# Kernel optimization log

Hardware: AMD Instinct MI355X
Metric: run time of the kernel (lower is better)

Reference implementation:

```python
import jax, jax.numpy as jnp
import numpy as np
from functools import partial

N_NODES = 50000
BN_EPS = 1e-5


def _renumber(src, dst, mask, n_nodes):
    # Faithful to extract_batch_edge_idx: kept edges are relabeled by the rank of
    # their node id among the sorted unique node ids APPEARING in kept edges.
    m = mask.astype(jnp.int32)
    appear = jnp.zeros(n_nodes, jnp.int32)
    appear = appear.at[src].max(m)
    appear = appear.at[dst].max(m)
    new_id = jnp.cumsum(appear) - 1  # rank of each appearing node id
    s = jnp.where(mask, new_id[src], 0)
    d = jnp.where(mask, new_id[dst], 0)
    return s, d


def _gcn_conv(x, W, b, src, dst, ew, n):
    # PyG GCNConv: linear, add self-loops, symmetric normalization, scatter-add.
    xw = x @ W                                   # [n, out]
    deg = jax.ops.segment_sum(ew, dst, num_segments=n) + 1.0  # +1 self loop
    dinv = jax.lax.rsqrt(deg)
    norm = dinv[src] * dinv[dst] * ew            # masked edges -> 0 weight
    agg = jax.ops.segment_sum(norm[:, None] * xw[src], dst, num_segments=n)
    agg = agg + (dinv * dinv)[:, None] * xw      # self-loop contribution
    return agg + b


def setup_inputs() -> dict:
    key = jax.random.key(0)
    ks = jax.random.split(key, 8)
    R, N, E, B = 3, N_NODES, 1000000, 2048
    inp, hid, out = 256, 512, 256
    features = jax.random.normal(ks[0], (R, N, inp), jnp.float32)
    W1 = jax.random.normal(ks[1], (inp, hid), jnp.float32) * (1.0 / np.sqrt(inp))
    b1 = jnp.zeros((hid,), jnp.float32)
    W2 = jax.random.normal(ks[2], (hid, out), jnp.float32) * (1.0 / np.sqrt(hid))
    b2 = jnp.zeros((out,), jnp.float32)
    gamma = jnp.ones((hid,), jnp.float32)
    beta = jnp.zeros((hid,), jnp.float32)
    edge_index = jax.random.randint(ks[3], (R, 2, E), 0, N, jnp.int64)
    # distinct, sorted batch node ids (torch code iterates node values)
    batch_nodes = jnp.sort(jax.random.permutation(ks[4], N)[:B]).astype(jnp.int64)
    return {"features": features, "W1": W1, "b1": b1, "W2": W2, "b2": b2,
            "gamma": gamma, "beta": beta, "edge_index": edge_index,
            "batch_nodes": batch_nodes}


def reference(features, W1, b1, W2, b2, gamma, beta, edge_index, batch_nodes):
    R, N, _ = features.shape
    B = batch_nodes.shape[0]
    in_batch = jnp.zeros(N, bool).at[batch_nodes].set(True)
    outs = []
    for r in range(R):  # small fixed relation count
        src, dst = edge_index[r, 0], edge_index[r, 1]
        mask = in_batch[src] & in_batch[dst]
        ew = mask.astype(features.dtype)
        s, d = _renumber(src, dst, mask, N)
        x = features[r, batch_nodes]             # [B, inp]
        h = _gcn_conv(x, W1, b1, s, d, ew, B)    # [B, hid]
        # BatchNorm1d (training mode: biased batch stats)
        mu = h.mean(axis=0)
        var = h.var(axis=0)
        h = (h - mu) * jax.lax.rsqrt(var + BN_EPS) * gamma + beta
        outs.append(_gcn_conv(h, W2, b2, s, d, ew, B))  # [B, out]
    stacked = jnp.stack(outs, axis=0)            # [R, B, out]
    return stacked.reshape(B, -1)                # row-major reshape, as torch
```

## Files before the change

kernel.cpp:

```cpp
#include <hip/hip_runtime.h>
#include <hip/hip_bf16.h>
#include <stdint.h>
#include <stddef.h>

#define RNUM   3
#define NNODES 50000
#define ENUM   1000000
#define BATCH  2048
#define INP    256
#define HID    512
#define OUTC   256
#define BN_EPS 1e-5f

typedef __bf16 bf16x8 __attribute__((ext_vector_type(8)));
typedef float  f32x4  __attribute__((ext_vector_type(4)));

__device__ inline unsigned short f2bf(float f) {
    union { float f; unsigned u; } c; c.f = f;
    unsigned u = c.u;
    return (unsigned short)((u + 0x7fffu + ((u >> 16) & 1u)) >> 16);
}

__device__ inline uint4 pack8(float4 a, float4 b) {
    uint4 r;
    r.x = (unsigned)f2bf(a.x) | ((unsigned)f2bf(a.y) << 16);
    r.y = (unsigned)f2bf(a.z) | ((unsigned)f2bf(a.w) << 16);
    r.z = (unsigned)f2bf(b.x) | ((unsigned)f2bf(b.y) << 16);
    r.w = (unsigned)f2bf(b.z) | ((unsigned)f2bf(b.w) << 16);
    return r;
}

__global__ __launch_bounds__(256) void k_wt(const float* __restrict__ W1,
                                            const float* __restrict__ W2,
                                            unsigned short* __restrict__ W1T,
                                            unsigned short* __restrict__ W2T) {
    __shared__ float T[32][33];
    int z = blockIdx.z;
    const float* W = z ? W2 : W1;
    unsigned short* WT = z ? W2T : W1T;
    int K = z ? HID : INP;
    int N = z ? OUTC : HID;
    int kt = blockIdx.y, nt = blockIdx.x;
    if (kt * 32 >= K || nt * 32 >= N) return;
    int tx = threadIdx.x & 31, ty = threadIdx.x >> 5;
#pragma unroll
    for (int j = 0; j < 4; ++j)
        T[ty + j * 8][tx] = W[(size_t)(kt * 32 + ty + j * 8) * N + nt * 32 + tx];
    __syncthreads();
#pragma unroll
    for (int j = 0; j < 4; ++j)
        WT[(size_t)(nt * 32 + ty + j * 8) * K + kt * 32 + tx] = f2bf(T[tx][ty + j * 8]);
}

__global__ void k_prep(const int* __restrict__ bn, int* __restrict__ inv,
                       int* __restrict__ appear, float* __restrict__ deg,
                       float* __restrict__ musum, float* __restrict__ sqsum,
                       int* __restrict__ kcount) {
    int i = blockIdx.x * blockDim.x + threadIdx.x;
    if (i < NNODES) {
        int lo = 0, hi = BATCH;
        while (lo < hi) { int mid = (lo + hi) >> 1; if (bn[mid] < i) lo = mid + 1; else hi = mid; }
        inv[i] = (lo < BATCH && bn[lo] == i) ? lo : -1;
    }
    if (i < RNUM * BATCH) { appear[i] = 0; deg[i] = 0.0f; }
    if (i < RNUM * HID)   { musum[i] = 0.0f; sqsum[i] = 0.0f; }
    if (i < RNUM)         kcount[i] = 0;
}

__global__ void k_mask(const int* __restrict__ edge_index, const int* __restrict__ inv,
                       int* __restrict__ appear, int2* __restrict__ edges,
                       int* __restrict__ kcount) {
    int z = blockIdx.z;
    const int* src = edge_index + (size_t)z * 2 * ENUM;
    const int* dst = src + ENUM;
    int2* ed = edges + (size_t)z * ENUM;
    int* app = appear + z * BATCH;
    int stride = gridDim.x * blockDim.x;
    for (int e4 = blockIdx.x * blockDim.x + threadIdx.x; e4 < ENUM / 4; e4 += stride) {
        int4 s4 = ((const int4*)src)[e4];
        int4 d4 = ((const int4*)dst)[e4];
        int ss[4] = {s4.x, s4.y, s4.z, s4.w};
        int dd[4] = {d4.x, d4.y, d4.z, d4.w};
#pragma unroll
        for (int i = 0; i < 4; ++i) {
            int ps = inv[ss[i]];
            int pd = inv[dd[i]];
            if (ps >= 0 && pd >= 0) {
                int idx = atomicAdd(kcount + z, 1);
                ed[idx] = make_int2(ps, pd);
                app[ps] = 1;
                app[pd] = 1;
            }
        }
    }
}

__global__ __launch_bounds__(1024) void k_scanDeg(const int* __restrict__ appear,
                                                  int2* __restrict__ edges,
                                                  const int* __restrict__ kcount,
                                                  float* __restrict__ deg) {
    __shared__ int buf[2][BATCH];
    __shared__ float degs[BATCH];
    int z = blockIdx.x;
    const int* ap = appear + z * BATCH;
    int2* ed = edges + (size_t)z * ENUM;
    float* dg = deg + z * BATCH;
    int t = threadIdx.x;
    buf[0][t] = ap[t];
    buf[0][t + 1024] = ap[t + 1024];
    degs[t] = 0.0f; degs[t + 1024] = 0.0f;
    __syncthreads();
    int cur = 0;
    for (int off = 1; off < BATCH; off <<= 1) {
        int nxt = cur ^ 1;
        int i1 = t, i2 = t + 1024;
        buf[nxt][i1] = buf[cur][i1] + (i1 >= off ? buf[cur][i1 - off] : 0);
        buf[nxt][i2] = buf[cur][i2] + (i2 >= off ? buf[cur][i2 - off] : 0);
        __syncthreads();
        cur = nxt;
    }
    int K = kcount[z];
    for (int e = t; e < K; e += 1024) {
        int2 E = ed[e];
        int s = buf[cur][E.x] - 1;
        int d = buf[cur][E.y] - 1;
        ed[e] = make_int2(s, d);
        atomicAdd(&degs[d], 1.0f);
    }
    __syncthreads();
    dg[t] = degs[t];
    dg[t + 1024] = degs[t + 1024];
}

__global__ __launch_bounds__(256) void k_gemm1(
    const float* __restrict__ features, const int* __restrict__ bn,
    const unsigned short* __restrict__ W1T, const float* __restrict__ b1,
    const float* __restrict__ deg, float* __restrict__ xw, float* __restrict__ hbase) {
    __shared__ __align__(16) unsigned short As[64][40];
    __shared__ __align__(16) unsigned short Bs[64][40];
    int z = blockIdx.z;
    const float* feat = features + (size_t)z * NNODES * INP;
    const float* dgz = deg + z * BATCH;
    float* xwz = xw + (size_t)z * BATCH * HID;
    float* hbz = hbase + (size_t)z * BATCH * HID;
    int m0 = blockIdx.y * 64, n0 = blockIdx.x * 64;
    int t = threadIdx.x;
    int ar = t >> 2, aq = t & 3;
    int grow = bn[m0 + ar];
    const float* aptr = feat + (size_t)grow * INP + aq * 8;
    const unsigned short* bptr = W1T + (size_t)(n0 + ar) * INP + aq * 8;

    int lane = t & 63, wave = t >> 6;
    int wm = (wave & 1) * 32, wn = (wave >> 1) * 32;
    int ml = lane & 15, quad = lane >> 4, q8 = quad * 8;

    f32x4 acc[2][2] = {};
    for (int k0 = 0; k0 < INP; k0 += 32) {
        float4 a0 = *(const float4*)(aptr + k0);
        float4 a1 = *(const float4*)(aptr + k0 + 4);
        uint4 bv = *(const uint4*)(bptr + k0);
        *(uint4*)&As[ar][aq * 8] = pack8(a0, a1);
        *(uint4*)&Bs[ar][aq * 8] = bv;
        __syncthreads();
        bf16x8 af[2], bfr[2];
#pragma unroll
        for (int mi = 0; mi < 2; ++mi) af[mi]  = *(const bf16x8*)&As[wm + mi * 16 + ml][q8];
#pragma unroll
        for (int ni = 0; ni < 2; ++ni) bfr[ni] = *(const bf16x8*)&Bs[wn + ni * 16 + ml][q8];
#pragma unroll
        for (int mi = 0; mi < 2; ++mi)
#pragma unroll
            for (int ni = 0; ni < 2; ++ni)
                acc[mi][ni] = __builtin_amdgcn_mfma_f32_16x16x32_bf16(af[mi], bfr[ni], acc[mi][ni], 0, 0, 0);
        __syncthreads();
    }
#pragma unroll
    for (int mi = 0; mi < 2; ++mi)
#pragma unroll
        for (int r = 0; r < 4; ++r) {
            int row = m0 + wm + mi * 16 + quad * 4 + r;
            float d2 = 1.0f / (dgz[row] + 1.0f);
#pragma unroll
            for (int ni = 0; ni < 2; ++ni) {
                int col = n0 + wn + ni * 16 + ml;
                float c = acc[mi][ni][r];
                xwz[(size_t)row * HID + col] = c;
                hbz[(size_t)row * HID + col] = d2 * c + b1[col];
            }
        }
}

__global__ __launch_bounds__(256) void k_gemm2(
    const float* __restrict__ hbase, const float* __restrict__ musum,
    const float* __restrict__ sqsum, const float* __restrict__ gamma,
    const float* __restrict__ beta, const unsigned short* __restrict__ W2T,
    const float* __restrict__ b2, const float* __restrict__ deg,
    float* __restrict__ yw, float* __restrict__ out) {
    __shared__ __align__(16) unsigned short As[64][40];
    __shared__ __align__(16) unsigned short Bs[64][40];
    __shared__ __align__(16) float gs[HID];
    __shared__ __align__(16) float ss_[HID];
    int z = blockIdx.z;
    const float* hz = hbase + (size_t)z * BATCH * HID;
    const float* dgz = deg + z * BATCH;
    float* ywz = yw + (size_t)z * BATCH * OUTC;
    float* oz = out + (size_t)z * BATCH * OUTC;
    int m0 = blockIdx.y * 64, n0 = blockIdx.x * 64;
    int t = threadIdx.x;

#pragma unroll
    for (int c = t; c < HID; c += 256) {
        float mu = musum[z * HID + c] * (1.0f / BATCH);
        float ex2 = sqsum[z * HID + c] * (1.0f / BATCH);
        float var = ex2 - mu * mu;
        float g = rsqrtf(var + BN_EPS) * gamma[c];
        gs[c] = g;
        ss_[c] = beta[c] - mu * g;
    }
    __syncthreads();

    int ar = t >> 2, aq = t & 3;
    const float* aptr = hz + (size_t)(m0 + ar) * HID + aq * 8;
    const unsigned short* bptr = W2T + (size_t)(n0 + ar) * HID + aq * 8;

    int lane = t & 63, wave = t >> 6;
    int wm = (wave & 1) * 32, wn = (wave >> 1) * 32;
    int ml = lane & 15, quad = lane >> 4, q8 = quad * 8;

    f32x4 acc[2][2] = {};
    for (int k0 = 0; k0 < HID; k0 += 32) {
        float4 h0 = *(const float4*)(aptr + k0);
        float4 h1 = *(const float4*)(aptr + k0 + 4);
        float4 g0 = *(const float4*)(gs + k0 + aq * 8);
        float4 g1 = *(const float4*)(gs + k0 + aq * 8 + 4);
        float4 s0 = *(const float4*)(ss_ + k0 + aq * 8);
        float4 s1 = *(const float4*)(ss_ + k0 + aq * 8 + 4);
        float4 a0 = make_float4(h0.x * g0.x + s0.x, h0.y * g0.y + s0.y,
                                h0.z * g0.z + s0.z, h0.w * g0.w + s0.w);
        float4 a1 = make_float4(h1.x * g1.x + s1.x, h1.y * g1.y + s1.y,
                                h1.z * g1.z + s1.z, h1.w * g1.w + s1.w);
        uint4 bv = *(const uint4*)(bptr + k0);
        *(uint4*)&As[ar][aq * 8] = pack8(a0, a1);
        *(uint4*)&Bs[ar][aq * 8] = bv;
        __syncthreads();
        bf16x8 af[2], bfr[2];
#pragma unroll
        for (int mi = 0; mi < 2; ++mi) af[mi]  = *(const bf16x8*)&As[wm + mi * 16 + ml][q8];
#pragma unroll
        for (int ni = 0; ni < 2; ++ni) bfr[ni] = *(const bf16x8*)&Bs[wn + ni * 16 + ml][q8];
#pragma unroll
        for (int mi = 0; mi < 2; ++mi)
#pragma unroll
            for (int ni = 0; ni < 2; ++ni)
                acc[mi][ni] = __builtin_amdgcn_mfma_f32_16x16x32_bf16(af[mi], bfr[ni], acc[mi][ni], 0, 0, 0);
        __syncthreads();
    }
#pragma unroll
    for (int mi = 0; mi < 2; ++mi)
#pragma unroll
        for (int r = 0; r < 4; ++r) {
            int row = m0 + wm + mi * 16 + quad * 4 + r;
            float d2 = 1.0f / (dgz[row] + 1.0f);
#pragma unroll
            for (int ni = 0; ni < 2; ++ni) {
                int col = n0 + wn + ni * 16 + ml;
                float c = acc[mi][ni][r];
                ywz[(size_t)row * OUTC + col] = c;
                oz[(size_t)row * OUTC + col] = d2 * c + b2[col];
            }
        }
}

__global__ void k_agg(const int2* __restrict__ edges, const int* __restrict__ kcount,
                      const float* __restrict__ deg, const float* __restrict__ src_mat,
                      float* __restrict__ dst_mat, int ncol) {
    int z = blockIdx.z;
    int K = kcount[z];
    const int2* ed = edges + (size_t)z * ENUM;
    const float* dgz = deg + z * BATCH;
    const float* sm = src_mat + (size_t)z * BATCH * ncol;
    float* dm = dst_mat + (size_t)z * BATCH * ncol;
    int nq = ncol >> 2;
    for (int e = blockIdx.x; e < K; e += gridDim.x) {
        int2 E = ed[e];
        float w = rsqrtf(dgz[E.x] + 1.0f) * rsqrtf(dgz[E.y] + 1.0f);
        const float4* srow = (const float4*)(sm + (size_t)E.x * ncol);
        float* drow = dm + (size_t)E.y * ncol;
        for (int q = threadIdx.x; q < nq; q += blockDim.x) {
            float4 v = srow[q];
            atomicAdd(&drow[q * 4 + 0], w * v.x);
            atomicAdd(&drow[q * 4 + 1], w * v.y);
            atomicAdd(&drow[q * 4 + 2], w * v.z);
            atomicAdd(&drow[q * 4 + 3], w * v.w);
        }
    }
}

__global__ __launch_bounds__(256) void k_bnstats(const float* __restrict__ hbase,
                                                 float* __restrict__ musum,
                                                 float* __restrict__ sqsum) {
    int z = blockIdx.z;
    const float* h = hbase + (size_t)z * BATCH * HID;
    int c0 = threadIdx.x;
    int r0 = blockIdx.x * 32;
    float s1a = 0, s2a = 0, s1b = 0, s2b = 0;
    for (int rr = 0; rr < 32; ++rr) {
        const float* row = h + (size_t)(r0 + rr) * HID;
        float va = row[c0];
        float vb = row[c0 + 256];
        s1a += va; s2a += va * va;
        s1b += vb; s2b += vb * vb;
    }
    atomicAdd(&musum[z * HID + c0], s1a);       atomicAdd(&sqsum[z * HID + c0], s2a);
    atomicAdd(&musum[z * HID + c0 + 256], s1b); atomicAdd(&sqsum[z * HID + c0 + 256], s2b);
}

extern "C" void kernel_launch(void* const* d_in, const int* in_sizes, int n_in,
                              void* d_out, int out_size, void* d_ws, size_t ws_size,
                              hipStream_t stream) {
    const float* features    = (const float*)d_in[0];
    const float* W1          = (const float*)d_in[1];
    const float* b1          = (const float*)d_in[2];
    const float* W2          = (const float*)d_in[3];
    const float* b2          = (const float*)d_in[4];
    const float* gamma       = (const float*)d_in[5];
    const float* beta        = (const float*)d_in[6];
    const int*   edge_index  = (const int*)d_in[7];
    const int*   batch_nodes = (const int*)d_in[8];
    float* out = (float*)d_out;

    char* p = (char*)d_ws;
    size_t cur = 0;
    auto alloc = [&](size_t bytes) {
        void* r = p + cur;
        cur = (cur + bytes + 255) & ~(size_t)255;
        return r;
    };
    int*   inv    = (int*)  alloc(NNODES * sizeof(int));
    int*   appear = (int*)  alloc(RNUM * BATCH * sizeof(int));
    int*   kcount = (int*)  alloc(RNUM * sizeof(int));
    float* deg    = (float*)alloc(RNUM * BATCH * sizeof(float));
    float* musum  = (float*)alloc(RNUM * HID * sizeof(float));
    float* sqsum  = (float*)alloc(RNUM * HID * sizeof(float));
    unsigned short* W1T = (unsigned short*)alloc((size_t)HID * INP * sizeof(unsigned short));
    unsigned short* W2T = (unsigned short*)alloc((size_t)OUTC * HID * sizeof(unsigned short));
    int2*  edges  = (int2*) alloc((size_t)RNUM * ENUM * sizeof(int2));
    float* xw     = (float*)alloc((size_t)RNUM * BATCH * HID * sizeof(float));
    float* hbase  = (float*)alloc((size_t)RNUM * BATCH * HID * sizeof(float));
    float* yw     = (float*)alloc((size_t)RNUM * BATCH * OUTC * sizeof(float));
    (void)ws_size; (void)in_sizes; (void)n_in; (void)out_size;

    k_wt<<<dim3(16, 16, 2), 256, 0, stream>>>(W1, W2, W1T, W2T);
    k_prep<<<(NNODES + 255) / 256, 256, 0, stream>>>(batch_nodes, inv, appear, deg,
                                                     musum, sqsum, kcount);
    k_mask<<<dim3(512, 1, RNUM), 256, 0, stream>>>(edge_index, inv, appear, edges, kcount);
    k_scanDeg<<<RNUM, 1024, 0, stream>>>(appear, edges, kcount, deg);

    k_gemm1<<<dim3(HID / 64, BATCH / 64, RNUM), 256, 0, stream>>>(
        features, batch_nodes, W1T, b1, deg, xw, hbase);
    k_agg<<<dim3(256, 1, RNUM), 256, 0, stream>>>(edges, kcount, deg, xw, hbase, HID);

    k_bnstats<<<dim3(64, 1, RNUM), 256, 0, stream>>>(hbase, musum, sqsum);

    k_gemm2<<<dim3(OUTC / 64, BATCH / 64, RNUM), 256, 0, stream>>>(
        hbase, musum, sqsum, gamma, beta, W2T, b2, deg, yw, out);
    k_agg<<<dim3(256, 1, RNUM), 256, 0, stream>>>(edges, kcount, deg, yw, out, OUTC);
}
```

Baseline: 365.6 us.

## Aggregate before linear layers, fold BN shift into correction vector, fuse stats

Reorders each GCN layer so neighbour aggregation runs on the narrower input (256 columns of features) before the first GEMM, and on the pre-BN hidden state before the second GEMM. The BatchNorm affine is applied through a per-node coefficient vector (sum of edge norms plus self-loop term) times shift@W2. BN statistics are now accumulated in the GEMM1 epilogue, so the separate stats pass and the second aggregation on GEMM outputs go away. Weight transpose and prep are merged into one launch that also zeroes the aggregation buffers. The cost is extra zero-fill traffic and a per-block 512-length dot product in GEMM2. The edge-parallel aggregations still rely on float atomics.

Measured after the change: 401.0 us. 9.7% more time.

```diff
diff --git a/kernel.cpp b/kernel.cpp
--- a/kernel.cpp
+++ b/kernel.cpp
@@ -30,41 +30,47 @@
     return r;
 }
 
-__global__ __launch_bounds__(256) void k_wt(const float* __restrict__ W1,
-                                            const float* __restrict__ W2,
-                                            unsigned short* __restrict__ W1T,
-                                            unsigned short* __restrict__ W2T) {
+__global__ __launch_bounds__(256) void k_prep(
+    const float* __restrict__ W1, const float* __restrict__ W2,
+    const int* __restrict__ bn,
+    unsigned short* __restrict__ W1T, unsigned short* __restrict__ W2T,
+    int* __restrict__ inv, int* __restrict__ appear, int* __restrict__ kcount,
+    float* __restrict__ musum, float* __restrict__ sqsum,
+    float* __restrict__ xa, float* __restrict__ ha) {
     __shared__ float T[32][33];
-    int z = blockIdx.z;
-    const float* W = z ? W2 : W1;
-    unsigned short* WT = z ? W2T : W1T;
-    int K = z ? HID : INP;
-    int N = z ? OUTC : HID;
-    int kt = blockIdx.y, nt = blockIdx.x;
-    if (kt * 32 >= K || nt * 32 >= N) return;
-    int tx = threadIdx.x & 31, ty = threadIdx.x >> 5;
-#pragma unroll
-    for (int j = 0; j < 4; ++j)
-        T[ty + j * 8][tx] = W[(size_t)(kt * 32 + ty + j * 8) * N + nt * 32 + tx];
-    __syncthreads();
-#pragma unroll
-    for (int j = 0; j < 4; ++j)
-        WT[(size_t)(nt * 32 + ty + j * 8) * K + kt * 32 + tx] = f2bf(T[tx][ty + j * 8]);
-}
-
-__global__ void k_prep(const int* __restrict__ bn, int* __restrict__ inv,
-                       int* __restrict__ appear, float* __restrict__ deg,
-                       float* __restrict__ musum, float* __restrict__ sqsum,
-                       int* __restrict__ kcount) {
-    int i = blockIdx.x * blockDim.x + threadIdx.x;
-    if (i < NNODES) {
+    const int bid = blockIdx.x, tid = threadIdx.x;
+    const int gid = bid * 256 + tid;
+    const int nth = gridDim.x * 256;
+
+    if (bid < 256) {
+        int z = bid >> 7, rem = bid & 127;
+        const float* W = z ? W2 : W1;
+        unsigned short* WT = z ? W2T : W1T;
+        int K = z ? HID : INP, N = z ? OUTC : HID;
+        int kt = z ? (rem >> 3) : (rem >> 4);
+        int nt = z ? (rem & 7) : (rem & 15);
+        int tx = tid & 31, ty = tid >> 5;
+#pragma unroll
+        for (int j = 0; j < 4; ++j)
+            T[ty + j * 8][tx] = W[(size_t)(kt * 32 + ty + j * 8) * N + nt * 32 + tx];
+        __syncthreads();
+#pragma unroll
+        for (int j = 0; j < 4; ++j)
+            WT[(size_t)(nt * 32 + ty + j * 8) * K + kt * 32 + tx] = f2bf(T[tx][ty + j * 8]);
+    }
+    if (gid < NNODES) {
         int lo = 0, hi = BATCH;
-        while (lo < hi) { int mid = (lo + hi) >> 1; if (bn[mid] < i) lo = mid + 1; else hi = mid; }
-        inv[i] = (lo < BATCH && bn[lo] == i) ? lo : -1;
-    }
-    if (i < RNUM * BATCH) { appear[i] = 0; deg[i] = 0.0f; }
-    if (i < RNUM * HID)   { musum[i] = 0.0f; sqsum[i] = 0.0f; }
-    if (i < RNUM)         kcount[i] = 0;
+        while (lo < hi) { int mid = (lo + hi) >> 1; if (bn[mid] < gid) lo = mid + 1; else hi = mid; }
+        inv[gid] = (lo < BATCH && bn[lo] == gid) ? lo : -1;
+    }
+    float4 z4 = make_float4(0.f, 0.f, 0.f, 0.f);
+    const int XA4 = RNUM * BATCH * INP / 4;
+    const int HA4 = RNUM * BATCH * HID / 4;
+    for (int i = gid; i < XA4; i += nth) ((float4*)xa)[i] = z4;
+    for (int i = gid; i < HA4; i += nth) ((float4*)ha)[i] = z4;
+    if (gid < RNUM * BATCH) appear[gid] = 0;
+    if (gid < RNUM * HID) { musum[gid] = 0.0f; sqsum[gid] = 0.0f; }
+    if (gid < RNUM) kcount[gid] = 0;
 }
 
 __global__ void k_mask(const int* __restrict__ edge_index, const int* __restrict__ inv,
@@ -98,17 +104,21 @@
 __global__ __launch_bounds__(1024) void k_scanDeg(const int* __restrict__ appear,
                                                   int2* __restrict__ edges,
                                                   const int* __restrict__ kcount,
-                                                  float* __restrict__ deg) {
+                                                  float* __restrict__ deg,
+                                                  float* __restrict__ cvec) {
     __shared__ int buf[2][BATCH];
     __shared__ float degs[BATCH];
+    __shared__ float cs[BATCH];
     int z = blockIdx.x;
     const int* ap = appear + z * BATCH;
     int2* ed = edges + (size_t)z * ENUM;
     float* dg = deg + z * BATCH;
+    float* cv = cvec + z * BATCH;
     int t = threadIdx.x;
     buf[0][t] = ap[t];
     buf[0][t + 1024] = ap[t + 1024];
     degs[t] = 0.0f; degs[t + 1024] = 0.0f;
+    cs[t] = 0.0f; cs[t + 1024] = 0.0f;
     __syncthreads();
     int cur = 0;
     for (int off = 1; off < BATCH; off <<= 1) {
@@ -127,27 +137,61 @@
         ed[e] = make_int2(s, d);
         atomicAdd(&degs[d], 1.0f);
     }
+    __threadfence_block();
+    __syncthreads();
+    for (int e = t; e < K; e += 1024) {
+        int2 E = ed[e];
+        atomicAdd(&cs[E.y], rsqrtf(degs[E.x] + 1.0f) * rsqrtf(degs[E.y] + 1.0f));
+    }
     __syncthreads();
     dg[t] = degs[t];
     dg[t + 1024] = degs[t + 1024];
+    cv[t] = cs[t] + 1.0f / (degs[t] + 1.0f);
+    cv[t + 1024] = cs[t + 1024] + 1.0f / (degs[t + 1024] + 1.0f);
+}
+
+__global__ void k_aggx(const int2* __restrict__ edges, const int* __restrict__ kcount,
+                       const float* __restrict__ deg, const float* __restrict__ features,
+                       const int* __restrict__ bn, float* __restrict__ xa) {
+    int z = blockIdx.z;
+    int K = kcount[z];
+    const int2* ed = edges + (size_t)z * ENUM;
+    const float* dgz = deg + z * BATCH;
+    const float* feat = features + (size_t)z * NNODES * INP;
+    float* xaz = xa + (size_t)z * BATCH * INP;
+    int slot = threadIdx.x >> 6, lane = threadIdx.x & 63;
+    for (int e = blockIdx.x * 4 + slot; e < K; e += gridDim.x * 4) {
+        int2 E = ed[e];
+        float w = rsqrtf(dgz[E.x] + 1.0f) * rsqrtf(dgz[E.y] + 1.0f);
+        const float4* srow = (const float4*)(feat + (size_t)bn[E.x] * INP);
+        float* drow = xaz + (size_t)E.y * INP;
+        float4 v = srow[lane];
+        atomicAdd(&drow[lane * 4 + 0], w * v.x);
+        atomicAdd(&drow[lane * 4 + 1], w * v.y);
+        atomicAdd(&drow[lane * 4 + 2], w * v.z);
+        atomicAdd(&drow[lane * 4 + 3], w * v.w);
+    }
 }
 
 __global__ __launch_bounds__(256) void k_gemm1(
     const float* __restrict__ features, const int* __restrict__ bn,
-    const unsigned short* __restrict__ W1T, const float* __restrict__ b1,
-    const float* __restrict__ deg, float* __restrict__ xw, float* __restrict__ hbase) {
+    const float* __restrict__ xa, const unsigned short* __restrict__ W1T,
+    const float* __restrict__ b1, const float* __restrict__ deg,
+    float* __restrict__ h, float* __restrict__ musum, float* __restrict__ sqsum) {
     __shared__ __align__(16) unsigned short As[64][40];
     __shared__ __align__(16) unsigned short Bs[64][40];
     int z = blockIdx.z;
     const float* feat = features + (size_t)z * NNODES * INP;
+    const float* xaz = xa + (size_t)z * BATCH * INP;
     const float* dgz = deg + z * BATCH;
-    float* xwz = xw + (size_t)z * BATCH * HID;
-    float* hbz = hbase + (size_t)z * BATCH * HID;
+    float* hz = h + (size_t)z * BATCH * HID;
     int m0 = blockIdx.y * 64, n0 = blockIdx.x * 64;
     int t = threadIdx.x;
     int ar = t >> 2, aq = t & 3;
     int grow = bn[m0 + ar];
-    const float* aptr = feat + (size_t)grow * INP + aq * 8;
+    const float* fptr = feat + (size_t)grow * INP + aq * 8;
+    const float* xptr = xaz + (size_t)(m0 + ar) * INP + aq * 8;
+    float d2row = 1.0f / (dgz[m0 + ar] + 1.0f);
     const unsigned short* bptr = W1T + (size_t)(n0 + ar) * INP + aq * 8;
 
     int lane = t & 63, wave = t >> 6;
@@ -156,8 +200,14 @@
 
     f32x4 acc[2][2] = {};
     for (int k0 = 0; k0 < INP; k0 += 32) {
-        float4 a0 = *(const float4*)(aptr + k0);
-        float4 a1 = *(const float4*)(aptr + k0 + 4);
+        float4 f0 = *(const float4*)(fptr + k0);
+        float4 f1 = *(const float4*)(fptr + k0 + 4);
+        float4 x0 = *(const float4*)(xptr + k0);
+        float4 x1 = *(const float4*)(xptr + k0 + 4);
+        float4 a0 = make_float4(x0.x + d2row * f0.x, x0.y + d2row * f0.y,
+                                x0.z + d2row * f0.z, x0.w + d2row * f0.w);
+        float4 a1 = make_float4(x1.x + d2row * f1.x, x1.y + d2row * f1.y,
+                                x1.z + d2row * f1.z, x1.w + d2row * f1.w);
         uint4 bv = *(const uint4*)(bptr + k0);
         *(uint4*)&As[ar][aq * 8] = pack8(a0, a1);
         *(uint4*)&Bs[ar][aq * 8] = bv;
@@ -175,35 +225,68 @@
         __syncthreads();
     }
 #pragma unroll
-    for (int mi = 0; mi < 2; ++mi)
-#pragma unroll
-        for (int r = 0; r < 4; ++r) {
-            int row = m0 + wm + mi * 16 + quad * 4 + r;
-            float d2 = 1.0f / (dgz[row] + 1.0f);
-#pragma unroll
-            for (int ni = 0; ni < 2; ++ni) {
-                int col = n0 + wn + ni * 16 + ml;
-                float c = acc[mi][ni][r];
-                xwz[(size_t)row * HID + col] = c;
-                hbz[(size_t)row * HID + col] = d2 * c + b1[col];
+    for (int ni = 0; ni < 2; ++ni) {
+        int col = n0 + wn + ni * 16 + ml;
+        float bcol = b1[col];
+        float p1 = 0.0f, p2 = 0.0f;
+#pragma unroll
+        for (int mi = 0; mi < 2; ++mi)
+#pragma unroll
+            for (int r = 0; r < 4; ++r) {
+                int row = m0 + wm + mi * 16 + quad * 4 + r;
+                float c = acc[mi][ni][r] + bcol;
+                hz[(size_t)row * HID + col] = c;
+                p1 += c; p2 += c * c;
             }
+        p1 += __shfl_xor(p1, 32); p1 += __shfl_xor(p1, 16);
+        p2 += __shfl_xor(p2, 32); p2 += __shfl_xor(p2, 16);
+        if (quad == 0) {
+            atomicAdd(&musum[z * HID + col], p1);
+            atomicAdd(&sqsum[z * HID + col], p2);
         }
+    }
+}
+
+__global__ void k_aggh(const int2* __restrict__ edges, const int* __restrict__ kcount,
+                       const float* __restrict__ deg, const float* __restrict__ h,
+                       float* __restrict__ ha) {
+    int z = blockIdx.z;
+    int K = kcount[z];
+    const int2* ed = edges + (size_t)z * ENUM;
+    const float* dgz = deg + z * BATCH;
+    const float* hz = h + (size_t)z * BATCH * HID;
+    float* haz = ha + (size_t)z * BATCH * HID;
+    int slot = threadIdx.x >> 7, lane = threadIdx.x & 127;
+    for (int e = blockIdx.x * 2 + slot; e < K; e += gridDim.x * 2) {
+        int2 E = ed[e];
+        float w = rsqrtf(dgz[E.x] + 1.0f) * rsqrtf(dgz[E.y] + 1.0f);
+        const float4* srow = (const float4*)(hz + (size_t)E.x * HID);
+        float* drow = haz + (size_t)E.y * HID;
+        float4 v = srow[lane];
+        atomicAdd(&drow[lane * 4 + 0], w * v.x);
+        atomicAdd(&drow[lane * 4 + 1], w * v.y);
+        atomicAdd(&drow[lane * 4 + 2], w * v.z);
+        atomicAdd(&drow[lane * 4 + 3], w * v.w);
+    }
 }
 
 __global__ __launch_bounds__(256) void k_gemm2(
-    const float* __restrict__ hbase, const float* __restrict__ musum,
-    const float* __restrict__ sqsum, const float* __restrict__ gamma,
-    const float* __restrict__ beta, const unsigned short* __restrict__ W2T,
+    const float* __restrict__ h, const float* __restrict__ ha,
+    const float* __restrict__ musum, const float* __restrict__ sqsum,
+    const float* __restrict__ gamma, const float* __restrict__ beta,
+    const float* __restrict__ W2, const unsigned short* __restrict__ W2T,
     const float* __restrict__ b2, const float* __restrict__ deg,
-    float* __restrict__ yw, float* __restrict__ out) {
+    const float* __restrict__ cvec, float* __restrict__ out) {
     __shared__ __align__(16) unsigned short As[64][40];
     __shared__ __align__(16) unsigned short Bs[64][40];
-    __shared__ __align__(16) float gs[HID];
-    __shared__ __align__(16) float ss_[HID];
+    __shared__ __align__(16) float gvec[HID];
+    __shared__ __align__(16) float svec[HID];
+    __shared__ __align__(16) float tvec[OUTC];
     int z = blockIdx.z;
-    const float* hz = hbase + (size_t)z * BATCH * HID;
+    const float* hz = h + (size_t)z * BATCH * HID;
+    const float* haz = ha + (size_t)z * BATCH * HID;
     const float* dgz = deg + z * BATCH;
-    float* ywz = yw + (size_t)z * BATCH * OUTC;
+    const float* cvz = cvec + z * BATCH;
     float* oz = out + (size_t)z * BATCH * OUTC;
     int m0 = blockIdx.y * 64, n0 = blockIdx.x * 64;
     int t = threadIdx.x;
@@ -214,13 +297,22 @@
         float ex2 = sqsum[z * HID + c] * (1.0f / BATCH);
         float var = ex2 - mu * mu;
         float g = rsqrtf(var + BN_EPS) * gamma[c];
-        gs[c] = g;
-        ss_[c] = beta[c] - mu * g;
+        gvec[c] = g;
+        svec[c] = beta[c] - mu * g;
     }
     __syncthreads();
+    {
+        float tc = 0.0f;
+#pragma unroll 4
+        for (int k = 0; k < HID; ++k) tc += svec[k] * W2[(size_t)k * OUTC + t];
+        tvec[t] = tc;
+    }
+    __syncthreads();
 
     int ar = t >> 2, aq = t & 3;
-    const float* aptr = hz + (size_t)(m0 + ar) * HID + aq * 8;
+    const float* haptr = haz + (size_t)(m0 + ar) * HID + aq * 8;
+    const float* hptr  = hz  + (size_t)(m0 + ar) * HID + aq * 8;
+    float d2row = 1.0f / (dgz[m0 + ar] + 1.0f);
     const unsigned short* bptr = W2T + (size_t)(n0 + ar) * HID + aq * 8;
 
     int lane = t & 63, wave = t >> 6;
@@ -229,16 +321,16 @@
 
     f32x4 acc[2][2] = {};
     for (int k0 = 0; k0 < HID; k0 += 32) {
-        float4 h0 = *(const float4*)(aptr + k0);
-        float4 h1 = *(const float4*)(aptr + k0 + 4);
-        float4 g0 = *(const float4*)(gs + k0 + aq * 8);
-        float4 g1 = *(const float4*)(gs + k0 + aq * 8 + 4);
-        float4 s0 = *(const float4*)(ss_ + k0 + aq * 8);
-        float4 s1 = *(const float4*)(ss_ + k0 + aq * 8 + 4);
-        float4 a0 = make_float4(h0.x * g0.x + s0.x, h0.y * g0.y + s0.y,
-                                h0.z * g0.z + s0.z, h0.w * g0.w + s0.w);
-        float4 a1 = make_float4(h1.x * g1.x + s1.x, h1.y * g1.y + s1.y,
-                                h1.z * g1.z + s1.z, h1.w * g1.w + s1.w);
+        float4 u0 = *(const float4*)(haptr + k0);
+        float4 u1 = *(const float4*)(haptr + k0 + 4);
+        float4 v0 = *(const float4*)(hptr + k0);
+        float4 v1 = *(const float4*)(hptr + k0 + 4);
+        float4 g0 = *(const float4*)(gvec + k0 + aq * 8);
+        float4 g1 = *(const float4*)(gvec + k0 + aq * 8 + 4);
+        float4 a0 = make_float4((u0.x + d2row * v0.x) * g0.x, (u0.y + d2row * v0.y) * g0.y,
+                                (u0.z + d2row * v0.z) * g0.z, (u0.w + d2row * v0.w) * g0.w);
+        float4 a1 = make_float4((u1.x + d2row * v1.x) * g1.x, (u1.y + d2row * v1.y) * g1.y,
+                                (u1.z + d2row * v1.z) * g1.z, (u1.w + d2row * v1.w) * g1.w);
         uint4 bv = *(const uint4*)(bptr + k0);
         *(uint4*)&As[ar][aq * 8] = pack8(a0, a1);
         *(uint4*)&Bs[ar][aq * 8] = bv;
@@ -260,59 +352,13 @@
 #pragma unroll
         for (int r = 0; r < 4; ++r) {
             int row = m0 + wm + mi * 16 + quad * 4 + r;
-            float d2 = 1.0f / (dgz[row] + 1.0f);
+            float cv = cvz[row];
 #pragma unroll
             for (int ni = 0; ni < 2; ++ni) {
                 int col = n0 + wn + ni * 16 + ml;
-                float c = acc[mi][ni][r];
-                ywz[(size_t)row * OUTC + col] = c;
-                oz[(size_t)row * OUTC + col] = d2 * c + b2[col];
+                oz[(size_t)row * OUTC + col] = acc[mi][ni][r] + cv * tvec[col] + b2[col];
             }
         }
-}
-
-__global__ void k_agg(const int2* __restrict__ edges, const int* __restrict__ kcount,
-                      const float* __restrict__ deg, const float* __restrict__ src_mat,
-                      float* __restrict__ dst_mat, int ncol) {
-    int z = blockIdx.z;
-    int K = kcount[z];
-    const int2* ed = edges + (size_t)z * ENUM;
-    const float* dgz = deg + z * BATCH;
-    const float* sm = src_mat + (size_t)z * BATCH * ncol;
-    float* dm = dst_mat + (size_t)z * BATCH * ncol;
-    int nq = ncol >> 2;
-    for (int e = blockIdx.x; e < K; e += gridDim.x) {
-        int2 E = ed[e];
-        float w = rsqrtf(dgz[E.x] + 1.0f) * rsqrtf(dgz[E.y] + 1.0f);
-        const float4* srow = (const float4*)(sm + (size_t)E.x * ncol);
-        float* drow = dm + (size_t)E.y * ncol;
-        for (int q = threadIdx.x; q < nq; q += blockDim.x) {
-            float4 v = srow[q];
-            atomicAdd(&drow[q * 4 + 0], w * v.x);
-            atomicAdd(&drow[q * 4 + 1], w * v.y);
-            atomicAdd(&drow[q * 4 + 2], w * v.z);
-            atomicAdd(&drow[q * 4 + 3], w * v.w);
-        }
-    }
-}
-
-__global__ __launch_bounds__(256) void k_bnstats(const float* __restrict__ hbase,
-                                                 float* __restrict__ musum,
-                                                 float* __restrict__ sqsum) {
-    int z = blockIdx.z;
-    const float* h = hbase + (size_t)z * BATCH * HID;
-    int c0 = threadIdx.x;
-    int r0 = blockIdx.x * 32;
-    float s1a = 0, s2a = 0, s1b = 0, s2b = 0;
-    for (int rr = 0; rr < 32; ++rr) {
-        const float* row = h + (size_t)(r0 + rr) * HID;
-        float va = row[c0];
-        float vb = row[c0 + 256];
-        s1a += va; s2a += va * va;
-        s1b += vb; s2b += vb * vb;
-    }
-    atomicAdd(&musum[z * HID + c0], s1a);       atomicAdd(&sqsum[z * HID + c0], s2a);
-    atomicAdd(&musum[z * HID + c0 + 256], s1b); atomicAdd(&sqsum[z * HID + c0 + 256], s2b);
 }
 
 extern "C" void kernel_launch(void* const* d_in, const int* in_sizes, int n_in,
@@ -340,29 +386,26 @@
     int*   appear = (int*)  alloc(RNUM * BATCH * sizeof(int));
     int*   kcount = (int*)  alloc(RNUM * sizeof(int));
     float* deg    = (float*)alloc(RNUM * BATCH * sizeof(float));
+    float* cvec   = (float*)alloc(RNUM * BATCH * sizeof(float));
     float* musum  = (float*)alloc(RNUM * HID * sizeof(float));
     float* sqsum  = (float*)alloc(RNUM * HID * sizeof(float));
     unsigned short* W1T = (unsigned short*)alloc((size_t)HID * INP * sizeof(unsigned short));
     unsigned short* W2T = (unsigned short*)alloc((size_t)OUTC * HID * sizeof(unsigned short));
     int2*  edges  = (int2*) alloc((size_t)RNUM * ENUM * sizeof(int2));
-    float* xw     = (float*)alloc((size_t)RNUM * BATCH * HID * sizeof(float));
-    float* hbase  = (float*)alloc((size_t)RNUM * BATCH * HID * sizeof(float));
-    float* yw     = (float*)alloc((size_t)RNUM * BATCH * OUTC * sizeof(float));
+    float* xa     = (float*)alloc((size_t)RNUM * BATCH * INP * sizeof(float));
+    float* ha     = (float*)alloc((size_t)RNUM * BATCH * HID * sizeof(float));
+    float* h      = (float*)alloc((size_t)RNUM * BATCH * HID * sizeof(float));
     (void)ws_size; (void)in_sizes; (void)n_in; (void)out_size;
 
-    k_wt<<<dim3(16, 16, 2), 256, 0, stream>>>(W1, W2, W1T, W2T);
-    k_prep<<<(NNODES + 255) / 256, 256, 0, stream>>>(batch_nodes, inv, appear, deg,
-                                                     musum, sqsum, kcount);
+    k_prep<<<1024, 256, 0, stream>>>(W1, W2, batch_nodes, W1T, W2T, inv, appear,
+                                     kcount, musum, sqsum, xa, ha);
     k_mask<<<dim3(512, 1, RNUM), 256, 0, stream>>>(edge_index, inv, appear, edges, kcount);
-    k_scanDeg<<<RNUM, 1024, 0, stream>>>(appear, edges, kcount, deg);
-
+    k_scanDeg<<<RNUM, 1024, 0, stream>>>(appear, edges, kcount, deg, cvec);
+    k_aggx<<<dim3(128, 1, RNUM), 256, 0, stream>>>(edges, kcount, deg, features,
+                                                   batch_nodes, xa);
     k_gemm1<<<dim3(HID / 64, BATCH / 64, RNUM), 256, 0, stream>>>(
-        features, batch_nodes, W1T, b1, deg, xw, hbase);
-    k_agg<<<dim3(256, 1, RNUM), 256, 0, stream>>>(edges, kcount, deg, xw, hbase, HID);
-
-    k_bnstats<<<dim3(64, 1, RNUM), 256, 0, stream>>>(hbase, musum, sqsum);
-
+        features, batch_nodes, xa, W1T, b1, deg, h, musum, sqsum);
+    k_aggh<<<dim3(256, 1, RNUM), 256, 0, stream>>>(edges, kcount, deg, h, ha);
     k_gemm2<<<dim3(OUTC / 64, BATCH / 64, RNUM), 256, 0, stream>>>(
-        hbase, musum, sqsum, gamma, beta, W2T, b2, deg, yw, out);
-    k_agg<<<dim3(256, 1, RNUM), 256, 0, stream>>>(edges, kcount, deg, yw, out, OUTC);
-}
+        h, ha, musum, sqsum, gamma, beta, W2, W2T, b2, deg, cvec, out);
+}
```
